# Performance work log

Hardware: AMD Instinct MI355X
Metric: run time of the kernel (lower is better)

Reference implementation:

```python
import jax, jax.numpy as jnp
import numpy as np

B, N = 16, 286
EMB_DIM = 4
CLOUD_DIM = 4
NB = 3          # number_of_basis
HID = 150       # radial MLP hidden width
RADIUS = 3.0    # neighbor radius / max_radius of cosine basis
FF = 512


def sp5(x):
    # torch Softplus(beta=5)
    return jax.nn.softplus(5.0 * x) / 5.0


def cosine_basis(r):
    # e3nn CosineBasisModel embedding: cos^2 bumps on [0, RADIUS]
    centers = jnp.linspace(0.0, RADIUS, NB)
    step = centers[1] - centers[0]
    d = (r[..., None] - centers) / step                     # [B,N,N,NB]
    return jnp.cos(jnp.pi / 2 * d) ** 2 * (jnp.abs(d) < 1.0)


def cloud_conv(feats, dist, mask, ws, bs, dim_out):
    # radial MLP on pairwise distances -> per-pair [dim_out, dim_in] kernel (l=0 only)
    x = cosine_basis(dist)
    for w, b in zip(ws[:-1], bs[:-1]):
        x = sp5(x @ w + b)
    R = x @ ws[-1] + bs[-1]                                 # [B,N,N,dim_out*dim_in]
    b_, n_ = dist.shape[0], dist.shape[1]
    k = R.reshape(b_, n_, n_, dim_out, -1) * mask[..., None, None]
    nb = jnp.maximum(mask.sum(-1), 1.0)                     # neighbors per atom [B,N]
    out = jnp.einsum('zabij,zbj->zai', k, feats) / jnp.sqrt(nb)[..., None]
    return out


def setup_inputs() -> dict:
    key = jax.random.key(0)
    ks = jax.random.split(key, 32)
    xyz = jax.random.normal(ks[0], (B, N, 3), dtype=jnp.float32)
    Z = jax.random.randint(ks[1], (B, N), 0, 11)
    emb = jax.random.normal(ks[2], (11, EMB_DIM), dtype=jnp.float32)
    inp = {'xyz': xyz, 'Z': Z, 'emb': emb}
    # radial MLPs per cloud: 3 -> 150 -> 150 -> 150 -> dim_out*dim_in (=16)
    dims = [NB, HID, HID, HID, CLOUD_DIM * CLOUD_DIM]
    ki = 3
    for c in range(2):
        for l in range(4):
            w = jax.random.normal(ks[ki], (dims[l], dims[l + 1]), dtype=jnp.float32) / np.sqrt(dims[l])
            b = jnp.zeros((dims[l + 1],), dtype=jnp.float32)
            inp[f'c{c}_w{l}'] = w
            inp[f'c{c}_b{l}'] = b
            ki += 1
    cloud_out = CLOUD_DIM * 2  # cloud_dim * cloud_order^2 * nclouds = 8
    inp['fc_w'] = jax.random.normal(ks[ki], (cloud_out, FF), dtype=jnp.float32) / np.sqrt(cloud_out); ki += 1
    inp['fc_b'] = jnp.zeros((FF,), dtype=jnp.float32)
    inp['bn_g'] = jnp.ones((FF,), dtype=jnp.float32)
    inp['bn_b'] = jnp.zeros((FF,), dtype=jnp.float32)
    inp['out_w'] = jax.random.normal(ks[ki], (FF, 1), dtype=jnp.float32) / np.sqrt(FF); ki += 1
    inp['out_b'] = jnp.zeros((1,), dtype=jnp.float32)
    return inp


def reference(xyz, Z, emb,
              c0_w0, c0_b0, c0_w1, c0_b1, c0_w2, c0_b2, c0_w3, c0_b3,
              c1_w0, c1_b0, c1_w1, c1_b1, c1_w2, c1_b2, c1_w3, c1_b3,
              fc_w, fc_b, bn_g, bn_b, out_w, out_b):
    feats = emb[Z]                                          # [B,N,emb_dim]
    diff = xyz[:, :, None, :] - xyz[:, None, :, :]
    dist = jnp.sqrt(jnp.sum(diff * diff, -1) + 1e-12)       # [B,N,N]
    mask = (dist < RADIUS).astype(feats.dtype)
    f1 = cloud_conv(feats, dist, mask,
                    [c0_w0, c0_w1, c0_w2, c0_w3], [c0_b0, c0_b1, c0_b2, c0_b3], CLOUD_DIM)
    f2 = cloud_conv(f1, dist, mask,
                    [c1_w0, c1_w1, c1_w2, c1_w3], [c1_b0, c1_b1, c1_b2, c1_b3], CLOUD_DIM)
    feats_cat = jnp.concatenate([f1, f2], axis=2)           # [B,N,8]
    # lp_pool2d(norm=2, kernel=(N,1)) == L2 norm over atom dim
    pooled = jnp.sqrt(jnp.sum(feats_cat ** 2, axis=1))      # [B,8]
    h = jax.nn.softplus(pooled @ fc_w + fc_b)
    mean = h.mean(0)
    var = h.var(0)
    h = jax.nn.softplus((h - mean) / jnp.sqrt(var + 1e-5) * bn_g + bn_b)
    return jax.nn.sigmoid(h @ out_w + out_b)[:, 0]          # [B]
```

## Files before the change

### kernel.cpp

```cpp
#include <hip/hip_runtime.h>
#include <hip/hip_bf16.h>
#include <hip/hip_fp16.h>
#include <math.h>

#define B_SZ   16
#define N_ATOM 286
#define NT     1024
#define HIDW   150
#define FF_DIM 512
#define WPAD   152
#define WROWS  151
#define BLK_PER_Z 72

__device__ __forceinline__ float softplus_f(float x) {
  return fmaxf(x, 0.0f) + log1pf(expf(-fabsf(x)));
}
__device__ __forceinline__ float sp5_f(float x) {
  float t = 5.0f * x;
  return (fmaxf(t, 0.0f) + log1pf(expf(-fabsf(t)))) * 0.2f;
}

__global__ __launch_bounds__(256) void prep_kernel(
    const float* __restrict__ w1a, const float* __restrict__ b1a,
    const float* __restrict__ w2a, const float* __restrict__ b2a,
    const float* __restrict__ w1c, const float* __restrict__ b1c,
    const float* __restrict__ w2c, const float* __restrict__ b2c,
    float* __restrict__ Wp) {
  const int m = blockIdx.y;
  const float* W  = (m == 0) ? w1a : (m == 1) ? w2a : (m == 2) ? w1c : w2c;
  const float* Bb = (m == 0) ? b1a : (m == 1) ? b2a : (m == 2) ? b1c : b2c;
  int idx = blockIdx.x * 256 + threadIdx.x;
  if (idx < WROWS * WPAD) {
    int i = idx / WPAD, o = idx % WPAD;
    float v = 0.0f;
    if (o < HIDW) v = (i < HIDW) ? W[i * HIDW + o] : Bb[o];
    Wp[(size_t)m * WROWS * WPAD + idx] = v;
  }
}

__global__ __launch_bounds__(256) void table_kernel(
    const float* __restrict__ a_w0, const float* __restrict__ a_b0,
    const float* __restrict__ a_w3, const float* __restrict__ a_b3,
    const float* __restrict__ c_w0, const float* __restrict__ c_b0,
    const float* __restrict__ c_w3, const float* __restrict__ c_b3,
    const float* __restrict__ Wp,
    __half* __restrict__ tabh0, __half* __restrict__ tabh1) {
  __shared__ float actA[WPAD * 8];
  __shared__ float actB[WPAD * 8];

  const int nblk = NT / 8;
  const int cloud = (blockIdx.x >= nblk) ? 1 : 0;
  const int blk   = blockIdx.x - cloud * nblk;
  const float* w0 = cloud ? c_w0 : a_w0;  const float* b0 = cloud ? c_b0 : a_b0;
  const float* w3 = cloud ? c_w3 : a_w3;  const float* b3 = cloud ? c_b3 : a_b3;
  const float* __restrict__ Wp1 = Wp + (size_t)(cloud * 2)     * WROWS * WPAD;
  const float* __restrict__ Wp2 = Wp + (size_t)(cloud * 2 + 1) * WROWS * WPAD;
  __half* table = cloud ? tabh1 : tabh0;

  const int tid  = threadIdx.x;
  const int lane = tid & 63;
  const int wave = __builtin_amdgcn_readfirstlane(tid >> 6);
  const int e0   = wave * 2;
  const int gbase = blk * 8;
  const int jj = (lane < 38) ? lane : 37;

  float x0[3], x1[3];
  #pragma unroll
  for (int k = 0; k < 3; ++k) {
    float r0 = 3.0f * (float)(gbase + e0)     / (float)(NT - 1);
    float r1 = 3.0f * (float)(gbase + e0 + 1) / (float)(NT - 1);
    float d0 = (r0 - 1.5f * (float)k) * (1.0f / 1.5f);
    float d1 = (r1 - 1.5f * (float)k) * (1.0f / 1.5f);
    float c0 = cosf(1.57079632679489662f * d0);
    float c1 = cosf(1.57079632679489662f * d1);
    x0[k] = (fabsf(d0) < 1.0f) ? c0 * c0 : 0.0f;
    x1[k] = (fabsf(d1) < 1.0f) ? c1 * c1 : 0.0f;
  }

  #pragma unroll
  for (int c = 0; c < 3; ++c) {
    int o = lane + 64 * c;
    int oc = (o < HIDW) ? o : (HIDW - 1);
    float w00 = w0[oc], w01 = w0[HIDW + oc], w02 = w0[2 * HIDW + oc], bb = b0[oc];
    float h0 = sp5_f(bb + x0[0] * w00 + x0[1] * w01 + x0[2] * w02);
    float h1 = sp5_f(bb + x1[0] * w00 + x1[1] * w01 + x1[2] * w02);
    if (o < HIDW) *(float2*)(&actA[o * 8 + e0]) = make_float2(h0, h1);
  }

  {
    const float* __restrict__ Wb = Wp1 + 4 * jj;
    float4 a0 = *(const float4*)(Wp1 + HIDW * WPAD + 4 * jj);
    float4 a1 = a0;
    #pragma unroll 10
    for (int i = 0; i < HIDW; ++i) {
      float4 wv = *(const float4*)(Wb + i * WPAD);
      float2 h  = *(const float2*)(&actA[i * 8 + e0]);
      a0.x = __builtin_fmaf(h.x, wv.x, a0.x); a1.x = __builtin_fmaf(h.y, wv.x, a1.x);
      a0.y = __builtin_fmaf(h.x, wv.y, a0.y); a1.y = __builtin_fmaf(h.y, wv.y, a1.y);
      a0.z = __builtin_fmaf(h.x, wv.z, a0.z); a1.z = __builtin_fmaf(h.y, wv.z, a1.z);
      a0.w = __builtin_fmaf(h.x, wv.w, a0.w); a1.w = __builtin_fmaf(h.y, wv.w, a1.w);
    }
    *(float2*)(&actB[(4 * jj + 0) * 8 + e0]) = make_float2(sp5_f(a0.x), sp5_f(a1.x));
    *(float2*)(&actB[(4 * jj + 1) * 8 + e0]) = make_float2(sp5_f(a0.y), sp5_f(a1.y));
    *(float2*)(&actB[(4 * jj + 2) * 8 + e0]) = make_float2(sp5_f(a0.z), sp5_f(a1.z));
    *(float2*)(&actB[(4 * jj + 3) * 8 + e0]) = make_float2(sp5_f(a0.w), sp5_f(a1.w));
  }

  {
    const float* __restrict__ Wb = Wp2 + 4 * jj;
    float4 a0 = *(const float4*)(Wp2 + HIDW * WPAD + 4 * jj);
    float4 a1 = a0;
    #pragma unroll 10
    for (int i = 0; i < HIDW; ++i) {
      float4 wv = *(const float4*)(Wb + i * WPAD);
      float2 h  = *(const float2*)(&actB[i * 8 + e0]);
      a0.x = __builtin_fmaf(h.x, wv.x, a0.x); a1.x = __builtin_fmaf(h.y, wv.x, a1.x);
      a0.y = __builtin_fmaf(h.x, wv.y, a0.y); a1.y = __builtin_fmaf(h.y, wv.y, a1.y);
      a0.z = __builtin_fmaf(h.x, wv.z, a0.z); a1.z = __builtin_fmaf(h.y, wv.z, a1.z);
      a0.w = __builtin_fmaf(h.x, wv.w, a0.w); a1.w = __builtin_fmaf(h.y, wv.w, a1.w);
    }
    *(float2*)(&actA[(4 * jj + 0) * 8 + e0]) = make_float2(sp5_f(a0.x), sp5_f(a1.x));
    *(float2*)(&actA[(4 * jj + 1) * 8 + e0]) = make_float2(sp5_f(a0.y), sp5_f(a1.y));
    *(float2*)(&actA[(4 * jj + 2) * 8 + e0]) = make_float2(sp5_f(a0.z), sp5_f(a1.z));
    *(float2*)(&actA[(4 * jj + 3) * 8 + e0]) = make_float2(sp5_f(a0.w), sp5_f(a1.w));
  }

  {
    const int o  = lane & 15;
    const int ig = lane >> 4;
    float a0 = 0.f, a1 = 0.f;
    for (int i = ig; i < HIDW; i += 4) {
      float wv = w3[i * 16 + o];
      float h0 = actA[i * 8 + e0];
      float h1 = actA[i * 8 + e0 + 1];
      a0 = __builtin_fmaf(h0, wv, a0);
      a1 = __builtin_fmaf(h1, wv, a1);
    }
    a0 += __shfl_xor(a0, 16, 64); a0 += __shfl_xor(a0, 32, 64);
    a1 += __shfl_xor(a1, 16, 64); a1 += __shfl_xor(a1, 32, 64);
    if (lane < 16) {
      float bb = b3[o];
      table[(size_t)(gbase + e0)     * 16 + o] = __float2half(a0 + bb);
      table[(size_t)(gbase + e0 + 1) * 16 + o] = __float2half(a1 + bb);
    }
  }
}

__device__ __forceinline__ void cvt8(uint4 q, float* out) {
  const __half2* h = (const __half2*)&q;
  #pragma unroll
  for (int k = 0; k < 4; ++k) {
    float2 f = __half22float2(h[k]);
    out[2 * k] = f.x; out[2 * k + 1] = f.y;
  }
}

__global__ __launch_bounds__(256) void conv_kernel(
    const float* __restrict__ xyz, const int* __restrict__ Z,
    const float* __restrict__ emb, const float* __restrict__ feats_in,
    const __half* __restrict__ tabh, float* __restrict__ f_out, int gather) {
  __shared__ float xs[N_ATOM], ys[N_ATOM], zs[N_ATOM];
  __shared__ float fxs[N_ATOM], fys[N_ATOM], fzs[N_ATOM], fws[N_ATOM];
  const int tid  = threadIdx.x;
  const int wave = tid >> 6;
  const int lane = tid & 63;
  const int z = blockIdx.x / BLK_PER_Z;
  const int a = (blockIdx.x % BLK_PER_Z) * 4 + wave;

  for (int b = tid; b < N_ATOM; b += 256) {
    const float* p = xyz + ((size_t)z * N_ATOM + b) * 3;
    xs[b] = p[0]; ys[b] = p[1]; zs[b] = p[2];
    float4 fb;
    if (gather) {
      int zi = Z[z * N_ATOM + b];
      fb = *(const float4*)(emb + (size_t)zi * 4);
    } else {
      fb = *(const float4*)(feats_in + ((size_t)z * N_ATOM + b) * 4);
    }
    fxs[b] = fb.x; fys[b] = fb.y; fzs[b] = fb.z; fws[b] = fb.w;
  }
  __syncthreads();
  if (a >= N_ATOM) return;

  const float ax = xs[a], ay = ys[a], az = zs[a];

  float acc[4] = {0.f, 0.f, 0.f, 0.f};
  float cnt = 0.f;
  for (int b = lane; b < N_ATOM; b += 64) {
    float dx = ax - xs[b], dy = ay - ys[b], dz = az - zs[b];
    float r = sqrtf(dx * dx + dy * dy + dz * dz + 1e-12f);
    float msk = (r < 3.0f) ? 1.0f : 0.0f;
    float t = r * ((float)(NT - 1) / 3.0f);
    int idx = (int)t;
    if (idx > NT - 2) idx = NT - 2;
    float fr = t - (float)idx;
    const uint4* Tp = (const uint4*)(tabh + (size_t)idx * 16);
    uint4 q0 = Tp[0], q1 = Tp[1], q2 = Tp[2], q3 = Tp[3];
    float fbx = fxs[b], fby = fys[b], fbz = fzs[b], fbw = fws[b];
    cnt += msk;
    float r0[16], r1[16];
    cvt8(q0, r0); cvt8(q1, r0 + 8);
    cvt8(q2, r1); cvt8(q3, r1 + 8);
    #pragma unroll
    for (int i = 0; i < 4; ++i) {
      float v0 = r0[4 * i + 0] + fr * (r1[4 * i + 0] - r0[4 * i + 0]);
      float v1 = r0[4 * i + 1] + fr * (r1[4 * i + 1] - r0[4 * i + 1]);
      float v2 = r0[4 * i + 2] + fr * (r1[4 * i + 2] - r0[4 * i + 2]);
      float v3 = r0[4 * i + 3] + fr * (r1[4 * i + 3] - r0[4 * i + 3]);
      acc[i] = __builtin_fmaf(msk, v0 * fbx + v1 * fby + v2 * fbz + v3 * fbw,
                              acc[i]);
    }
  }
  #pragma unroll
  for (int m = 32; m > 0; m >>= 1) {
    #pragma unroll
    for (int i = 0; i < 4; ++i) acc[i] += __shfl_xor(acc[i], m, 64);
    cnt += __shfl_xor(cnt, m, 64);
  }
  if (lane == 0) {
    float nb = cnt < 1.0f ? 1.0f : cnt;
    float sc = 1.0f / sqrtf(nb);
    float4 o;
    o.x = acc[0] * sc; o.y = acc[1] * sc; o.z = acc[2] * sc; o.w = acc[3] * sc;
    *(float4*)(f_out + ((size_t)z * N_ATOM + a) * 4) = o;
  }
}

__global__ __launch_bounds__(256) void pool_kernel(
    const float* __restrict__ f1, const float* __restrict__ f2,
    float* __restrict__ pool_sq) {
  __shared__ float red[4][8];
  const int z = blockIdx.x;
  const int tid = threadIdx.x;
  const int lane = tid & 63, wave = tid >> 6;
  float s[8] = {0.f, 0.f, 0.f, 0.f, 0.f, 0.f, 0.f, 0.f};
  for (int a = tid; a < N_ATOM; a += 256) {
    float4 v1 = *(const float4*)(f1 + ((size_t)z * N_ATOM + a) * 4);
    float4 v2 = *(const float4*)(f2 + ((size_t)z * N_ATOM + a) * 4);
    s[0] += v1.x * v1.x; s[1] += v1.y * v1.y;
    s[2] += v1.z * v1.z; s[3] += v1.w * v1.w;
    s[4] += v2.x * v2.x; s[5] += v2.y * v2.y;
    s[6] += v2.z * v2.z; s[7] += v2.w * v2.w;
  }
  #pragma unroll
  for (int m = 32; m > 0; m >>= 1) {
    #pragma unroll
    for (int k = 0; k < 8; ++k) s[k] += __shfl_xor(s[k], m, 64);
  }
  if (lane == 0) {
    #pragma unroll
    for (int k = 0; k < 8; ++k) red[wave][k] = s[k];
  }
  __syncthreads();
  if (tid < 8)
    pool_sq[z * 8 + tid] = red[0][tid] + red[1][tid] + red[2][tid] + red[3][tid];
}

__global__ __launch_bounds__(512) void tail_kernel(
    const float* __restrict__ pool_sq,
    const float* __restrict__ fc_w, const float* __restrict__ fc_b,
    const float* __restrict__ bn_g, const float* __restrict__ bn_b,
    const float* __restrict__ out_w, const float* __restrict__ out_b,
    float* __restrict__ out) {
  __shared__ float pooled[16][8];
  __shared__ float part[8][16];
  const int tid = threadIdx.x;

  if (tid < 128) pooled[tid >> 3][tid & 7] = sqrtf(pool_sq[tid]);
  __syncthreads();

  const int f = tid;
  float hv[16];
  float mean = 0.f;
  #pragma unroll
  for (int z = 0; z < 16; ++z) {
    float a = fc_b[f];
    #pragma unroll
    for (int c = 0; c < 8; ++c) a += pooled[z][c] * fc_w[c * FF_DIM + f];
    hv[z] = softplus_f(a);
    mean += hv[z];
  }
  mean *= (1.0f / 16.0f);
  float var = 0.f;
  #pragma unroll
  for (int z = 0; z < 16; ++z) { float d = hv[z] - mean; var += d * d; }
  var *= (1.0f / 16.0f);
  float istd = 1.0f / sqrtf(var + 1e-5f);
  float g = bn_g[f], bb = bn_b[f], ow = out_w[f];
  float contrib[16];
  #pragma unroll
  for (int z = 0; z < 16; ++z)
    contrib[z] = softplus_f((hv[z] - mean) * istd * g + bb) * ow;

  const int lane = tid & 63, wv = tid >> 6;
  #pragma unroll
  for (int m = 32; m > 0; m >>= 1) {
    #pragma unroll
    for (int z = 0; z < 16; ++z) contrib[z] += __shfl_xor(contrib[z], m, 64);
  }
  if (lane == 0) {
    #pragma unroll
    for (int z = 0; z < 16; ++z) part[wv][z] = contrib[z];
  }
  __syncthreads();
  if (tid < 16) {
    float s = out_b[0];
    #pragma unroll
    for (int w8 = 0; w8 < 8; ++w8) s += part[w8][tid];
    out[tid] = 1.0f / (1.0f + expf(-s));
  }
}

extern "C" void kernel_launch(void* const* d_in, const int* in_sizes, int n_in,
                              void* d_out, int out_size, void* d_ws, size_t ws_size,
                              hipStream_t stream) {
  const float* xyz = (const float*)d_in[0];
  const int*   Z   = (const int*)d_in[1];
  const float* emb = (const float*)d_in[2];
  const float* c0[8]; const float* c1[8];
  for (int i = 0; i < 8; ++i) {
    c0[i] = (const float*)d_in[3 + i];
    c1[i] = (const float*)d_in[11 + i];
  }
  const float* fc_w  = (const float*)d_in[19];
  const float* fc_b  = (const float*)d_in[20];
  const float* bn_g  = (const float*)d_in[21];
  const float* bn_b  = (const float*)d_in[22];
  const float* out_w = (const float*)d_in[23];
  const float* out_b = (const float*)d_in[24];
  float* out = (float*)d_out;

  float* wsf = (float*)d_ws;
  float* Wp = wsf;
  float* f1 = Wp + (size_t)4 * WROWS * WPAD;
  float* f2 = f1 + (size_t)B_SZ * N_ATOM * 4;
  float* pool_sq = f2 + (size_t)B_SZ * N_ATOM * 4;
  __half* tabh0 = (__half*)(pool_sq + 128);
  __half* tabh1 = tabh0 + (size_t)NT * 16;

  {
    dim3 g((WROWS * WPAD + 255) / 256, 4);
    prep_kernel<<<g, 256, 0, stream>>>(c0[2], c0[3], c0[4], c0[5],
                                       c1[2], c1[3], c1[4], c1[5], Wp);
  }

  table_kernel<<<2 * (NT / 8), 256, 0, stream>>>(
      c0[0], c0[1], c0[6], c0[7],
      c1[0], c1[1], c1[6], c1[7],
      Wp, tabh0, tabh1);

  const int conv_blocks = B_SZ * BLK_PER_Z;
  conv_kernel<<<conv_blocks, 256, 0, stream>>>(xyz, Z, emb, (const float*)nullptr,
                                               tabh0, f1, 1);
  conv_kernel<<<conv_blocks, 256, 0, stream>>>(xyz, Z, emb, f1,
                                               tabh1, f2, 0);

  pool_kernel<<<B_SZ, 256, 0, stream>>>(f1, f2, pool_sq);

  tail_kernel<<<1, 512, 0, stream>>>(pool_sq, fc_w, fc_b, bn_g, bn_b,
                                     out_w, out_b, out);
}
```

Baseline: 180.1 us.

## Drop weight-prep kernel and split table MLP reduction across waves

Removes the separate prep kernel that padded and bias-augmented the hidden-layer weights, so the table kernel reads the raw weights directly. Each block now handles 2 table entries instead of 8, and the hidden dimension is split across the 4 waves with partial sums reduced through shared memory. The aim is to cut one kernel launch and spread the table work over four times as many blocks. In exchange it adds several __syncthreads, re-reads the weights per block with 8-byte rather than 16-byte loads, and each weight fetch now serves only 2 entries.

```diff
diff --git a/kernel.cpp b/kernel.cpp
--- a/kernel.cpp
+++ b/kernel.cpp
@@ -1,5 +1,4 @@
 #include <hip/hip_runtime.h>
-#include <hip/hip_bf16.h>
 #include <hip/hip_fp16.h>
 #include <math.h>
 
@@ -8,8 +7,6 @@
 #define NT     1024
 #define HIDW   150
 #define FF_DIM 512
-#define WPAD   152
-#define WROWS  151
 #define BLK_PER_Z 72
 
 __device__ __forceinline__ float softplus_f(float x) {
@@ -20,129 +17,153 @@
   return (fmaxf(t, 0.0f) + log1pf(expf(-fabsf(t)))) * 0.2f;
 }
 
-__global__ __launch_bounds__(256) void prep_kernel(
-    const float* __restrict__ w1a, const float* __restrict__ b1a,
-    const float* __restrict__ w2a, const float* __restrict__ b2a,
-    const float* __restrict__ w1c, const float* __restrict__ b1c,
-    const float* __restrict__ w2c, const float* __restrict__ b2c,
-    float* __restrict__ Wp) {
-  const int m = blockIdx.y;
-  const float* W  = (m == 0) ? w1a : (m == 1) ? w2a : (m == 2) ? w1c : w2c;
-  const float* Bb = (m == 0) ? b1a : (m == 1) ? b2a : (m == 2) ? b1c : b2c;
-  int idx = blockIdx.x * 256 + threadIdx.x;
-  if (idx < WROWS * WPAD) {
-    int i = idx / WPAD, o = idx % WPAD;
-    float v = 0.0f;
-    if (o < HIDW) v = (i < HIDW) ? W[i * HIDW + o] : Bb[o];
-    Wp[(size_t)m * WROWS * WPAD + idx] = v;
-  }
-}
-
 __global__ __launch_bounds__(256) void table_kernel(
     const float* __restrict__ a_w0, const float* __restrict__ a_b0,
+    const float* __restrict__ a_w1, const float* __restrict__ a_b1,
+    const float* __restrict__ a_w2, const float* __restrict__ a_b2,
     const float* __restrict__ a_w3, const float* __restrict__ a_b3,
     const float* __restrict__ c_w0, const float* __restrict__ c_b0,
+    const float* __restrict__ c_w1, const float* __restrict__ c_b1,
+    const float* __restrict__ c_w2, const float* __restrict__ c_b2,
     const float* __restrict__ c_w3, const float* __restrict__ c_b3,
-    const float* __restrict__ Wp,
     __half* __restrict__ tabh0, __half* __restrict__ tabh1) {
-  __shared__ float actA[WPAD * 8];
-  __shared__ float actB[WPAD * 8];
-
-  const int nblk = NT / 8;
+  __shared__ float actA[304];
+  __shared__ float actB[304];
+  __shared__ float part[4 * 304];
+
+  const int nblk = NT / 2;
   const int cloud = (blockIdx.x >= nblk) ? 1 : 0;
   const int blk   = blockIdx.x - cloud * nblk;
   const float* w0 = cloud ? c_w0 : a_w0;  const float* b0 = cloud ? c_b0 : a_b0;
+  const float* w1 = cloud ? c_w1 : a_w1;  const float* b1 = cloud ? c_b1 : a_b1;
+  const float* w2 = cloud ? c_w2 : a_w2;  const float* b2 = cloud ? c_b2 : a_b2;
   const float* w3 = cloud ? c_w3 : a_w3;  const float* b3 = cloud ? c_b3 : a_b3;
-  const float* __restrict__ Wp1 = Wp + (size_t)(cloud * 2)     * WROWS * WPAD;
-  const float* __restrict__ Wp2 = Wp + (size_t)(cloud * 2 + 1) * WROWS * WPAD;
   __half* table = cloud ? tabh1 : tabh0;
 
   const int tid  = threadIdx.x;
   const int lane = tid & 63;
   const int wave = __builtin_amdgcn_readfirstlane(tid >> 6);
-  const int e0   = wave * 2;
-  const int gbase = blk * 8;
+  const int gbase = blk * 2;
+
+  const int i0 = wave * 38;
+  const int i1 = (i0 + 38 < HIDW) ? i0 + 38 : HIDW;
   const int jj = (lane < 38) ? lane : 37;
-
-  float x0[3], x1[3];
-  #pragma unroll
-  for (int k = 0; k < 3; ++k) {
-    float r0 = 3.0f * (float)(gbase + e0)     / (float)(NT - 1);
-    float r1 = 3.0f * (float)(gbase + e0 + 1) / (float)(NT - 1);
-    float d0 = (r0 - 1.5f * (float)k) * (1.0f / 1.5f);
-    float d1 = (r1 - 1.5f * (float)k) * (1.0f / 1.5f);
-    float c0 = cosf(1.57079632679489662f * d0);
-    float c1 = cosf(1.57079632679489662f * d1);
-    x0[k] = (fabsf(d0) < 1.0f) ? c0 * c0 : 0.0f;
-    x1[k] = (fabsf(d1) < 1.0f) ? c1 * c1 : 0.0f;
-  }
-
-  #pragma unroll
-  for (int c = 0; c < 3; ++c) {
-    int o = lane + 64 * c;
-    int oc = (o < HIDW) ? o : (HIDW - 1);
-    float w00 = w0[oc], w01 = w0[HIDW + oc], w02 = w0[2 * HIDW + oc], bb = b0[oc];
-    float h0 = sp5_f(bb + x0[0] * w00 + x0[1] * w01 + x0[2] * w02);
-    float h1 = sp5_f(bb + x1[0] * w00 + x1[1] * w01 + x1[2] * w02);
-    if (o < HIDW) *(float2*)(&actA[o * 8 + e0]) = make_float2(h0, h1);
-  }
+  const int cA = 4 * jj;
+  const int cB = (cA + 2 < HIDW) ? cA + 2 : 148;
+
+  if (tid < HIDW) {
+    float w00 = w0[tid], w01 = w0[HIDW + tid], w02 = w0[2 * HIDW + tid];
+    float bb = b0[tid];
+    #pragma unroll
+    for (int e = 0; e < 2; ++e) {
+      float r = 3.0f * (float)(gbase + e) / (float)(NT - 1);
+      float acc = bb;
+      #pragma unroll
+      for (int k = 0; k < 3; ++k) {
+        float d = (r - 1.5f * (float)k) * (1.0f / 1.5f);
+        float c = cosf(1.57079632679489662f * d);
+        float x = (fabsf(d) < 1.0f) ? c * c : 0.0f;
+        acc += x * ((k == 0) ? w00 : (k == 1) ? w01 : w02);
+      }
+      actA[tid * 2 + e] = sp5_f(acc);
+    }
+  }
+  __syncthreads();
 
   {
-    const float* __restrict__ Wb = Wp1 + 4 * jj;
-    float4 a0 = *(const float4*)(Wp1 + HIDW * WPAD + 4 * jj);
-    float4 a1 = a0;
-    #pragma unroll 10
-    for (int i = 0; i < HIDW; ++i) {
-      float4 wv = *(const float4*)(Wb + i * WPAD);
-      float2 h  = *(const float2*)(&actA[i * 8 + e0]);
-      a0.x = __builtin_fmaf(h.x, wv.x, a0.x); a1.x = __builtin_fmaf(h.y, wv.x, a1.x);
-      a0.y = __builtin_fmaf(h.x, wv.y, a0.y); a1.y = __builtin_fmaf(h.y, wv.y, a1.y);
-      a0.z = __builtin_fmaf(h.x, wv.z, a0.z); a1.z = __builtin_fmaf(h.y, wv.z, a1.z);
-      a0.w = __builtin_fmaf(h.x, wv.w, a0.w); a1.w = __builtin_fmaf(h.y, wv.w, a1.w);
-    }
-    *(float2*)(&actB[(4 * jj + 0) * 8 + e0]) = make_float2(sp5_f(a0.x), sp5_f(a1.x));
-    *(float2*)(&actB[(4 * jj + 1) * 8 + e0]) = make_float2(sp5_f(a0.y), sp5_f(a1.y));
-    *(float2*)(&actB[(4 * jj + 2) * 8 + e0]) = make_float2(sp5_f(a0.z), sp5_f(a1.z));
-    *(float2*)(&actB[(4 * jj + 3) * 8 + e0]) = make_float2(sp5_f(a0.w), sp5_f(a1.w));
-  }
+    float a00 = 0.f, a01 = 0.f, a10 = 0.f, a11 = 0.f;
+    float a20 = 0.f, a21 = 0.f, a30 = 0.f, a31 = 0.f;
+    #pragma unroll 4
+    for (int i = i0; i < i1; ++i) {
+      float2 wA = *(const float2*)(w1 + i * HIDW + cA);
+      float2 wB = *(const float2*)(w1 + i * HIDW + cB);
+      float2 h  = *(const float2*)(&actA[i * 2]);
+      a00 = __builtin_fmaf(h.x, wA.x, a00); a01 = __builtin_fmaf(h.y, wA.x, a01);
+      a10 = __builtin_fmaf(h.x, wA.y, a10); a11 = __builtin_fmaf(h.y, wA.y, a11);
+      a20 = __builtin_fmaf(h.x, wB.x, a20); a21 = __builtin_fmaf(h.y, wB.x, a21);
+      a30 = __builtin_fmaf(h.x, wB.y, a30); a31 = __builtin_fmaf(h.y, wB.y, a31);
+    }
+    if (lane < 38) {
+      float* p = &part[wave * 304];
+      *(float2*)(&p[(cA + 0) * 2]) = make_float2(a00, a01);
+      *(float2*)(&p[(cA + 1) * 2]) = make_float2(a10, a11);
+      if (jj < 37) {
+        *(float2*)(&p[(cB + 0) * 2]) = make_float2(a20, a21);
+        *(float2*)(&p[(cB + 1) * 2]) = make_float2(a30, a31);
+      }
+    }
+  }
+  __syncthreads();
+  if (tid < HIDW) {
+    float bb = b1[tid];
+    #pragma unroll
+    for (int e = 0; e < 2; ++e) {
+      float v = bb + part[0 * 304 + tid * 2 + e] + part[1 * 304 + tid * 2 + e]
+                   + part[2 * 304 + tid * 2 + e] + part[3 * 304 + tid * 2 + e];
+      actB[tid * 2 + e] = sp5_f(v);
+    }
+  }
+  __syncthreads();
 
   {
-    const float* __restrict__ Wb = Wp2 + 4 * jj;
-    float4 a0 = *(const float4*)(Wp2 + HIDW * WPAD + 4 * jj);
-    float4 a1 = a0;
-    #pragma unroll 10
-    for (int i = 0; i < HIDW; ++i) {
-      float4 wv = *(const float4*)(Wb + i * WPAD);
-      float2 h  = *(const float2*)(&actB[i * 8 + e0]);
-      a0.x = __builtin_fmaf(h.x, wv.x, a0.x); a1.x = __builtin_fmaf(h.y, wv.x, a1.x);
-      a0.y = __builtin_fmaf(h.x, wv.y, a0.y); a1.y = __builtin_fmaf(h.y, wv.y, a1.y);
-      a0.z = __builtin_fmaf(h.x, wv.z, a0.z); a1.z = __builtin_fmaf(h.y, wv.z, a1.z);
-      a0.w = __builtin_fmaf(h.x, wv.w, a0.w); a1.w = __builtin_fmaf(h.y, wv.w, a1.w);
-    }
-    *(float2*)(&actA[(4 * jj + 0) * 8 + e0]) = make_float2(sp5_f(a0.x), sp5_f(a1.x));
-    *(float2*)(&actA[(4 * jj + 1) * 8 + e0]) = make_float2(sp5_f(a0.y), sp5_f(a1.y));
-    *(float2*)(&actA[(4 * jj + 2) * 8 + e0]) = make_float2(sp5_f(a0.z), sp5_f(a1.z));
-    *(float2*)(&actA[(4 * jj + 3) * 8 + e0]) = make_float2(sp5_f(a0.w), sp5_f(a1.w));
-  }
+    float a00 = 0.f, a01 = 0.f, a10 = 0.f, a11 = 0.f;
+    float a20 = 0.f, a21 = 0.f, a30 = 0.f, a31 = 0.f;
+    #pragma unroll 4
+    for (int i = i0; i < i1; ++i) {
+      float2 wA = *(const float2*)(w2 + i * HIDW + cA);
+      float2 wB = *(const float2*)(w2 + i * HIDW + cB);
+      float2 h  = *(const float2*)(&actB[i * 2]);
+      a00 = __builtin_fmaf(h.x, wA.x, a00); a01 = __builtin_fmaf(h.y, wA.x, a01);
+      a10 = __builtin_fmaf(h.x, wA.y, a10); a11 = __builtin_fmaf(h.y, wA.y, a11);
+      a20 = __builtin_fmaf(h.x, wB.x, a20); a21 = __builtin_fmaf(h.y, wB.x, a21);
+      a30 = __builtin_fmaf(h.x, wB.y, a30); a31 = __builtin_fmaf(h.y, wB.y, a31);
+    }
+    if (lane < 38) {
+      float* p = &part[wave * 304];
+      *(float2*)(&p[(cA + 0) * 2]) = make_float2(a00, a01);
+      *(float2*)(&p[(cA + 1) * 2]) = make_float2(a10, a11);
+      if (jj < 37) {
+        *(float2*)(&p[(cB + 0) * 2]) = make_float2(a20, a21);
+        *(float2*)(&p[(cB + 1) * 2]) = make_float2(a30, a31);
+      }
+    }
+  }
+  __syncthreads();
+  if (tid < HIDW) {
+    float bb = b2[tid];
+    #pragma unroll
+    for (int e = 0; e < 2; ++e) {
+      float v = bb + part[0 * 304 + tid * 2 + e] + part[1 * 304 + tid * 2 + e]
+                   + part[2 * 304 + tid * 2 + e] + part[3 * 304 + tid * 2 + e];
+      actA[tid * 2 + e] = sp5_f(v);
+    }
+  }
+  __syncthreads();
 
   {
     const int o  = lane & 15;
     const int ig = lane >> 4;
-    float a0 = 0.f, a1 = 0.f;
-    for (int i = ig; i < HIDW; i += 4) {
+    float p0 = 0.f, p1 = 0.f;
+    for (int i = i0 + ig; i < i1; i += 4) {
       float wv = w3[i * 16 + o];
-      float h0 = actA[i * 8 + e0];
-      float h1 = actA[i * 8 + e0 + 1];
-      a0 = __builtin_fmaf(h0, wv, a0);
-      a1 = __builtin_fmaf(h1, wv, a1);
-    }
-    a0 += __shfl_xor(a0, 16, 64); a0 += __shfl_xor(a0, 32, 64);
-    a1 += __shfl_xor(a1, 16, 64); a1 += __shfl_xor(a1, 32, 64);
+      float h0 = actA[i * 2 + 0];
+      float h1 = actA[i * 2 + 1];
+      p0 = __builtin_fmaf(h0, wv, p0);
+      p1 = __builtin_fmaf(h1, wv, p1);
+    }
+    p0 += __shfl_xor(p0, 16, 64); p0 += __shfl_xor(p0, 32, 64);
+    p1 += __shfl_xor(p1, 16, 64); p1 += __shfl_xor(p1, 32, 64);
     if (lane < 16) {
-      float bb = b3[o];
-      table[(size_t)(gbase + e0)     * 16 + o] = __float2half(a0 + bb);
-      table[(size_t)(gbase + e0 + 1) * 16 + o] = __float2half(a1 + bb);
-    }
+      part[wave * 32 + lane * 2 + 0] = p0;
+      part[wave * 32 + lane * 2 + 1] = p1;
+    }
+  }
+  __syncthreads();
+  if (tid < 32) {
+    int o = tid >> 1, e = tid & 1;
+    float v = b3[o] + part[0 * 32 + o * 2 + e] + part[1 * 32 + o * 2 + e]
+                    + part[2 * 32 + o * 2 + e] + part[3 * 32 + o * 2 + e];
+    table[(size_t)(gbase + e) * 16 + o] = __float2half(v);
   }
 }
 
@@ -331,23 +352,16 @@
   float* out = (float*)d_out;
 
   float* wsf = (float*)d_ws;
-  float* Wp = wsf;
-  float* f1 = Wp + (size_t)4 * WROWS * WPAD;
+  float* f1 = wsf;
   float* f2 = f1 + (size_t)B_SZ * N_ATOM * 4;
   float* pool_sq = f2 + (size_t)B_SZ * N_ATOM * 4;
   __half* tabh0 = (__half*)(pool_sq + 128);
   __half* tabh1 = tabh0 + (size_t)NT * 16;
 
-  {
-    dim3 g((WROWS * WPAD + 255) / 256, 4);
-    prep_kernel<<<g, 256, 0, stream>>>(c0[2], c0[3], c0[4], c0[5],
-                                       c1[2], c1[3], c1[4], c1[5], Wp);
-  }
-
-  table_kernel<<<2 * (NT / 8), 256, 0, stream>>>(
-      c0[0], c0[1], c0[6], c0[7],
-      c1[0], c1[1], c1[6], c1[7],
-      Wp, tabh0, tabh1);
+  table_kernel<<<2 * (NT / 2), 256, 0, stream>>>(
+      c0[0], c0[1], c0[2], c0[3], c0[4], c0[5], c0[6], c0[7],
+      c1[0], c1[1], c1[2], c1[3], c1[4], c1[5], c1[6], c1[7],
+      tabh0, tabh1);
 
   const int conv_blocks = B_SZ * BLK_PER_Z;
   conv_kernel<<<conv_blocks, 256, 0, stream>>>(xyz, Z, emb, (const float*)nullptr,
```

After: 166.0 us. 7.8% less time.
